# Performance work log

Measured on AMD Instinct MI355X. Metric: run time of the kernel, lower is better.

The kernel has to match this reference:

```python
import jax, jax.numpy as jnp
import numpy as np
import math

D_IN = 1024
D_OUT = 1024
NUM_HEADS = 16
D_HEAD = D_IN // NUM_HEADS


def setup_inputs() -> dict:
    key = jax.random.key(0)
    k1, k2, k3 = jax.random.split(key, 3)
    x = jax.random.normal(k1, (4, 2048, D_IN), dtype=jnp.float32)
    W_qkv = jax.random.normal(k2, (D_IN, 3 * D_OUT), dtype=jnp.float32) * (1.0 / math.sqrt(D_IN))
    b_qkv = jax.random.normal(k3, (3 * D_OUT,), dtype=jnp.float32) * 0.01
    return {"x": x, "W_qkv": W_qkv, "b_qkv": b_qkv}


def reference(x, W_qkv, b_qkv):
    B, S, _ = x.shape
    H, Dh = NUM_HEADS, D_HEAD
    # QKV projection: [B, S, 3*d_out]
    qkv = jnp.einsum('bsd,de->bse', x, W_qkv) + b_qkv
    # reshape per original: (B, S, H, 3*Dh) -> (B, H, S, 3*Dh)
    qkv = qkv.reshape(B, S, H, 3 * Dh).transpose(0, 2, 1, 3)
    q, k, v = jnp.split(qkv, 3, axis=-1)  # each [B, H, S, Dh]
    scale = 1.0 / math.sqrt(Dh)
    scores = jnp.einsum('bhqd,bhkd->bhqk', q, k) * scale
    attn = jax.nn.softmax(scores, axis=-1)
    ctx = jnp.einsum('bhqk,bhkd->bhqd', attn, v)  # [B, H, S, Dh]
    # (B, H, S, Dh) -> (B, S, H*Dh)
    return ctx.transpose(0, 2, 1, 3).reshape(B, S, D_OUT)
```

## Files before the change

kernel.cpp:

```cpp
#include <hip/hip_runtime.h>
#include <stdint.h>
#include <math.h>

#define D_IN   1024
#define NQKV   3072
#define NHEADS 16
#define DH     64
#define BATCH  4
#define SEQ    2048
#define MTOT   (BATCH*SEQ)

typedef __bf16    bf16x8 __attribute__((ext_vector_type(8)));
typedef _Float16  f16x8  __attribute__((ext_vector_type(8)));
typedef float     f32x4  __attribute__((ext_vector_type(4)));

__device__ __forceinline__ unsigned short f2bf(float f) {
    union { float f; uint32_t u; } c; c.f = f;
    uint32_t u = c.u;
    uint32_t r = u + 0x7fffu + ((u >> 16) & 1u);
    return (unsigned short)(r >> 16);
}
__device__ __forceinline__ float bf2f(unsigned short b) {
    union { uint32_t u; float f; } c; c.u = ((uint32_t)b) << 16;
    return c.f;
}
__device__ __forceinline__ uint32_t pkh(float a, float b) {
    auto h = __builtin_amdgcn_cvt_pkrtz(a, b);
    uint32_t u;
    __builtin_memcpy(&u, &h, 4);
    return u;
}

__global__ void k_convert_x(const float* __restrict__ x, unsigned short* __restrict__ xb) {
    int i = blockIdx.x * 256 + threadIdx.x;
    float4 v = ((const float4*)x)[i];
    ushort4 o;
    o.x = f2bf(v.x); o.y = f2bf(v.y); o.z = f2bf(v.z); o.w = f2bf(v.w);
    ((ushort4*)xb)[i] = o;
}

__global__ void k_convert_wt(const float* __restrict__ W, unsigned short* __restrict__ Wt) {
    __shared__ float tile[32][33];
    int tx = threadIdx.x, ty = threadIdx.y;
    int n0 = blockIdx.x * 32, k0 = blockIdx.y * 32;
    #pragma unroll
    for (int i = 0; i < 4; ++i) {
        int k = k0 + ty + i*8;
        tile[ty + i*8][tx] = W[(size_t)k * NQKV + n0 + tx];
    }
    __syncthreads();
    #pragma unroll
    for (int i = 0; i < 4; ++i) {
        int n = n0 + ty + i*8;
        Wt[(size_t)n * D_IN + k0 + tx] = f2bf(tile[tx][ty + i*8]);
    }
}

__global__ __launch_bounds__(256) void k_gemm_qkv(
    const unsigned short* __restrict__ A,
    const unsigned short* __restrict__ Bt,
    const float* __restrict__ bias,
    unsigned short* __restrict__ C)
{
    __shared__ __align__(16) unsigned short As[128*40];
    __shared__ __align__(16) unsigned short Bs[128*40];
    const int t = threadIdx.x;
    const int wave = t >> 6, lane = t & 63, quad = lane >> 4, l15 = lane & 15;
    const int wm = wave >> 1, wn = wave & 1;
    const int m0 = blockIdx.y * 128, n0 = blockIdx.x * 128;

    f32x4 acc[4][4] = {};

    for (int k0 = 0; k0 < D_IN; k0 += 32) {
        __syncthreads();
        #pragma unroll
        for (int i = 0; i < 2; ++i) {
            int idx = t + i*256;
            int row = idx >> 2, c = (idx & 3) << 3;
            *(uint4*)(&As[row*40 + c]) = *(const uint4*)(&A [(size_t)(m0+row)*D_IN + k0 + c]);
            *(uint4*)(&Bs[row*40 + c]) = *(const uint4*)(&Bt[(size_t)(n0+row)*D_IN + k0 + c]);
        }
        __syncthreads();
        bf16x8 a[4], b[4];
        #pragma unroll
        for (int tm = 0; tm < 4; ++tm)
            a[tm] = *(const bf16x8*)(&As[(wm*64 + tm*16 + l15)*40 + quad*8]);
        #pragma unroll
        for (int tn = 0; tn < 4; ++tn)
            b[tn] = *(const bf16x8*)(&Bs[(wn*64 + tn*16 + l15)*40 + quad*8]);
        #pragma unroll
        for (int tm = 0; tm < 4; ++tm)
            #pragma unroll
            for (int tn = 0; tn < 4; ++tn)
                acc[tm][tn] = __builtin_amdgcn_mfma_f32_16x16x32_bf16(a[tm], b[tn], acc[tm][tn], 0, 0, 0);
    }
    #pragma unroll
    for (int tn = 0; tn < 4; ++tn) {
        int col = n0 + wn*64 + tn*16 + l15;
        float bv = bias[col];
        #pragma unroll
        for (int tm = 0; tm < 4; ++tm) {
            #pragma unroll
            for (int r = 0; r < 4; ++r) {
                int row = m0 + wm*64 + tm*16 + quad*4 + r;
                C[(size_t)row*NQKV + col] = f2bf(acc[tm][tn][r] + bv);
            }
        }
    }
}

#define TP 66
__global__ __launch_bounds__(256) void k_transpose_v(
    const unsigned short* __restrict__ qkv,
    unsigned short* __restrict__ vtg)
{
    __shared__ unsigned short T[64*TP];
    const int t = threadIdx.x;
    const int bh = blockIdx.y, b = bh >> 4, h = bh & 15;
    const int s0 = blockIdx.x * 64;
    const unsigned short* src = qkv + (size_t)(b*SEQ + s0)*NQKV + h*(3*DH) + 2*DH;
    #pragma unroll
    for (int i = 0; i < 2; ++i) {
        int idx = t + i*256;
        int s = idx >> 3, c = (idx & 7) << 3;
        uint4 v = *(const uint4*)(src + (size_t)s*NQKV + c);
        unsigned short* dst = &T[s*TP + c];
        const unsigned short* pv = (const unsigned short*)&v;
        #pragma unroll
        for (int j = 0; j < 8; ++j) {
            _Float16 hv = (_Float16)bf2f(pv[j]);
            dst[j] = *(unsigned short*)&hv;
        }
    }
    __syncthreads();
    unsigned short* out = vtg + (size_t)bh * DH * SEQ + s0;
    #pragma unroll
    for (int i = 0; i < 16; ++i) {
        int idx = t + i*256;
        int d = idx >> 6, s = idx & 63;
        out[(size_t)d * SEQ + s] = T[s*TP + d];
    }
}

#define PPAD 40
#define OPAD 72
__global__ __launch_bounds__(256, 2) void k_attn(
    const unsigned short* __restrict__ qkv,
    const unsigned short* __restrict__ vtg,
    float* __restrict__ out)
{
    __shared__ __align__(16) unsigned short Pl[4*64*PPAD];
    __shared__ __align__(16) unsigned short Os[4*64*OPAD];
    __shared__ float Lp[4*64];

    const int t = threadIdx.x;
    const int wave = t >> 6, lane = t & 63, quad = lane >> 4, l15 = lane & 15;
    const int bh = blockIdx.y, b = bh >> 4, h = bh & 15;
    const int m0 = blockIdx.x * 64;
    const unsigned short* base  = qkv + (size_t)(b*SEQ)*NQKV + h*(3*DH);
    const unsigned short* kbase = base + DH;
    const unsigned short* vbase = vtg + (size_t)bh * DH * SEQ;

    bf16x8 qb[4][2];
    #pragma unroll
    for (int tq = 0; tq < 4; ++tq) {
        const unsigned short* qrow = base + (size_t)(m0 + tq*16 + l15) * NQKV;
        qb[tq][0] = *(const bf16x8*)(qrow + quad*8);
        qb[tq][1] = *(const bf16x8*)(qrow + 32 + quad*8);
    }

    f32x4 o[4][4] = {};
    float lp[4] = {0.f, 0.f, 0.f, 0.f};
    unsigned short* pw = &Pl[wave*64*PPAD];
    const float c = 0.125f * 1.44269504089f;

    bf16x8 kf[2][2][2];
    f16x8  vf[2][4];
    {
        int key0 = wave*32;
        #pragma unroll
        for (int tk = 0; tk < 2; ++tk) {
            const unsigned short* kr = kbase + (size_t)(key0 + tk*16 + l15)*NQKV;
            kf[0][tk][0] = *(const bf16x8*)(kr + quad*8);
            kf[0][tk][1] = *(const bf16x8*)(kr + 32 + quad*8);
        }
        #pragma unroll
        for (int td = 0; td < 4; ++td)
            vf[0][td] = *(const f16x8*)(vbase + (size_t)(td*16 + l15)*SEQ + key0 + quad*8);
    }

    #pragma unroll 2
    for (int it = 0; it < 16; ++it) {
        const int cur = it & 1, nxt = cur ^ 1;
        if (it < 15) {
            int key0 = (it+1)*128 + wave*32;
            #pragma unroll
            for (int tk = 0; tk < 2; ++tk) {
                const unsigned short* kr = kbase + (size_t)(key0 + tk*16 + l15)*NQKV;
                kf[nxt][tk][0] = *(const bf16x8*)(kr + quad*8);
                kf[nxt][tk][1] = *(const bf16x8*)(kr + 32 + quad*8);
            }
            #pragma unroll
            for (int td = 0; td < 4; ++td)
                vf[nxt][td] = *(const f16x8*)(vbase + (size_t)(td*16 + l15)*SEQ + key0 + quad*8);
        }
        #pragma unroll
        for (int tk = 0; tk < 2; ++tk) {
            #pragma unroll
            for (int tq = 0; tq < 4; ++tq) {
                f32x4 a = {};
                a = __builtin_amdgcn_mfma_f32_16x16x32_bf16(kf[cur][tk][0], qb[tq][0], a, 0, 0, 0);
                a = __builtin_amdgcn_mfma_f32_16x16x32_bf16(kf[cur][tk][1], qb[tq][1], a, 0, 0, 0);
                float p0 = exp2f(a[0]*c), p1 = exp2f(a[1]*c);
                float p2 = exp2f(a[2]*c), p3 = exp2f(a[3]*c);
                lp[tq] += (p0 + p1) + (p2 + p3);
                uint2 u; u.x = pkh(p0, p1); u.y = pkh(p2, p3);
                *(uint2*)(&pw[(tq*16 + l15)*PPAD + tk*16 + quad*4]) = u;
            }
        }
        f16x8 pb[4];
        #pragma unroll
        for (int tq = 0; tq < 4; ++tq)
            pb[tq] = *(const f16x8*)(&pw[(tq*16 + l15)*PPAD + quad*8]);
        #pragma unroll
        for (int td = 0; td < 4; ++td)
            #pragma unroll
            for (int tq = 0; tq < 4; ++tq)
                o[td][tq] = __builtin_amdgcn_mfma_f32_16x16x32_f16(vf[cur][td], pb[tq], o[td][tq], 0, 0, 0);
    }

    {
        unsigned short* ow = &Os[wave*64*OPAD];
        #pragma unroll
        for (int td = 0; td < 4; ++td)
            #pragma unroll
            for (int tq = 0; tq < 4; ++tq) {
                uint2 u; u.x = pkh(o[td][tq][0], o[td][tq][1]); u.y = pkh(o[td][tq][2], o[td][tq][3]);
                *(uint2*)(&ow[(tq*16 + l15)*OPAD + td*16 + quad*4]) = u;
            }
        #pragma unroll
        for (int tq = 0; tq < 4; ++tq) {
            float s = lp[tq];
            s += __shfl_xor(s, 16);
            s += __shfl_xor(s, 32);
            if (quad == 0) Lp[wave*64 + tq*16 + l15] = s;
        }
    }
    __syncthreads();
    float* outb = out + (size_t)(b*SEQ + m0) * (NHEADS*DH) + h*DH;
    #pragma unroll
    for (int i = 0; i < 16; ++i) {
        int idx = t + i*256;
        int q = idx >> 6, d = idx & 63;
        float lt = Lp[q] + Lp[64 + q] + Lp[128 + q] + Lp[192 + q];
        float s = 0.f;
        #pragma unroll
        for (int w2 = 0; w2 < 4; ++w2) {
            _Float16 hv = *(const _Float16*)&Os[(w2*64 + q)*OPAD + d];
            s += (float)hv;
        }
        outb[(size_t)q * (NHEADS*DH) + d] = s / lt;
    }
}

extern "C" void kernel_launch(void* const* d_in, const int* in_sizes, int n_in,
                              void* d_out, int out_size, void* d_ws, size_t ws_size,
                              hipStream_t stream) {
    const float* x    = (const float*)d_in[0];
    const float* W    = (const float*)d_in[1];
    const float* bias = (const float*)d_in[2];
    float* out = (float*)d_out;

    unsigned short* xb  = (unsigned short*)d_ws;
    unsigned short* Wt  = xb  + (size_t)MTOT * D_IN;
    unsigned short* qkv = Wt  + (size_t)NQKV * D_IN;
    unsigned short* vtg = xb;

    hipLaunchKernelGGL(k_convert_x,   dim3(MTOT*D_IN/4/256), dim3(256),    0, stream, x, xb);
    hipLaunchKernelGGL(k_convert_wt,  dim3(NQKV/32, D_IN/32), dim3(32, 8), 0, stream, W, Wt);
    hipLaunchKernelGGL(k_gemm_qkv,    dim3(NQKV/128, MTOT/128), dim3(256), 0, stream, xb, Wt, bias, qkv);
    hipLaunchKernelGGL(k_transpose_v, dim3(SEQ/64, BATCH*NHEADS), dim3(256), 0, stream, qkv, vtg);
    hipLaunchKernelGGL(k_attn,        dim3(SEQ/64, BATCH*NHEADS), dim3(256), 0, stream, qkv, vtg, out);
}
```

Before: 319.8 us.

## Use direct global-to-LDS loads in QKV GEMM, fold softmax scale, raise attention occupancy

The QKV GEMM now stages A and B tiles with global_load_lds, which writes straight into an unpadded LDS layout and skips the register round-trip. The softmax scale and log2e factor are folded into Q during the GEMM epilogue, so the attention kernel drops one multiply per score. The attention kernel merges its P and O scratch buffers into one LDS array, adding a barrier so P is no longer in use before O overwrites it. It also raises launch bounds to 4 blocks per CU to increase occupancy, at the risk of register spills. Removing the LDS padding may cause bank conflicts on the fragment reads, and Q is now rounded to bf16 after scaling, which slightly changes precision.

```diff
diff --git a/kernel.cpp b/kernel.cpp
--- a/kernel.cpp
+++ b/kernel.cpp
@@ -14,6 +14,9 @@
 typedef _Float16  f16x8  __attribute__((ext_vector_type(8)));
 typedef float     f32x4  __attribute__((ext_vector_type(4)));
 
+typedef __attribute__((address_space(3))) unsigned short       lds_us;
+typedef __attribute__((address_space(1))) const unsigned short glb_us;
+
 __device__ __forceinline__ unsigned short f2bf(float f) {
     union { float f; uint32_t u; } c; c.f = f;
     uint32_t u = c.u;
@@ -62,48 +65,55 @@
     const float* __restrict__ bias,
     unsigned short* __restrict__ C)
 {
-    __shared__ __align__(16) unsigned short As[128*40];
-    __shared__ __align__(16) unsigned short Bs[128*40];
+    __shared__ __align__(16) unsigned short As[128*32];
+    __shared__ __align__(16) unsigned short Bs[128*32];
     const int t = threadIdx.x;
     const int wave = t >> 6, lane = t & 63, quad = lane >> 4, l15 = lane & 15;
     const int wm = wave >> 1, wn = wave & 1;
     const int m0 = blockIdx.y * 128, n0 = blockIdx.x * 128;
+    const int crow = lane >> 2;
+    const int ccol = (lane & 3) << 3;
 
     f32x4 acc[4][4] = {};
+    lds_us* As3 = (lds_us*)As;
+    lds_us* Bs3 = (lds_us*)Bs;
 
     for (int k0 = 0; k0 < D_IN; k0 += 32) {
-        __syncthreads();
-        #pragma unroll
-        for (int i = 0; i < 2; ++i) {
-            int idx = t + i*256;
-            int row = idx >> 2, c = (idx & 3) << 3;
-            *(uint4*)(&As[row*40 + c]) = *(const uint4*)(&A [(size_t)(m0+row)*D_IN + k0 + c]);
-            *(uint4*)(&Bs[row*40 + c]) = *(const uint4*)(&Bt[(size_t)(n0+row)*D_IN + k0 + c]);
+        #pragma unroll
+        for (int j = 0; j < 2; ++j) {
+            int chunk = wave*2 + j;
+            const unsigned short* ga = A  + (size_t)(m0 + chunk*16 + crow)*D_IN + k0 + ccol;
+            const unsigned short* gb = Bt + (size_t)(n0 + chunk*16 + crow)*D_IN + k0 + ccol;
+            __builtin_amdgcn_global_load_lds((glb_us*)ga, As3 + chunk*512, 16, 0, 0);
+            __builtin_amdgcn_global_load_lds((glb_us*)gb, Bs3 + chunk*512, 16, 0, 0);
         }
         __syncthreads();
         bf16x8 a[4], b[4];
         #pragma unroll
         for (int tm = 0; tm < 4; ++tm)
-            a[tm] = *(const bf16x8*)(&As[(wm*64 + tm*16 + l15)*40 + quad*8]);
+            a[tm] = *(const bf16x8*)(&As[(wm*64 + tm*16 + l15)*32 + quad*8]);
         #pragma unroll
         for (int tn = 0; tn < 4; ++tn)
-            b[tn] = *(const bf16x8*)(&Bs[(wn*64 + tn*16 + l15)*40 + quad*8]);
+            b[tn] = *(const bf16x8*)(&Bs[(wn*64 + tn*16 + l15)*32 + quad*8]);
         #pragma unroll
         for (int tm = 0; tm < 4; ++tm)
             #pragma unroll
             for (int tn = 0; tn < 4; ++tn)
                 acc[tm][tn] = __builtin_amdgcn_mfma_f32_16x16x32_bf16(a[tm], b[tn], acc[tm][tn], 0, 0, 0);
-    }
+        __syncthreads();
+    }
+    const float qs = 0.125f * 1.44269504089f;
     #pragma unroll
     for (int tn = 0; tn < 4; ++tn) {
         int col = n0 + wn*64 + tn*16 + l15;
         float bv = bias[col];
+        float s = ((col % 192) < 64) ? qs : 1.0f;
         #pragma unroll
         for (int tm = 0; tm < 4; ++tm) {
             #pragma unroll
             for (int r = 0; r < 4; ++r) {
                 int row = m0 + wm*64 + tm*16 + quad*4 + r;
-                C[(size_t)row*NQKV + col] = f2bf(acc[tm][tn][r] + bv);
+                C[(size_t)row*NQKV + col] = f2bf((acc[tm][tn][r] + bv) * s);
             }
         }
     }
@@ -144,13 +154,12 @@
 
 #define PPAD 40
 #define OPAD 72
-__global__ __launch_bounds__(256, 2) void k_attn(
+__global__ __launch_bounds__(256, 4) void k_attn(
     const unsigned short* __restrict__ qkv,
     const unsigned short* __restrict__ vtg,
     float* __restrict__ out)
 {
-    __shared__ __align__(16) unsigned short Pl[4*64*PPAD];
-    __shared__ __align__(16) unsigned short Os[4*64*OPAD];
+    __shared__ __align__(16) unsigned short PO[4*64*OPAD];
     __shared__ float Lp[4*64];
 
     const int t = threadIdx.x;
@@ -171,8 +180,7 @@
 
     f32x4 o[4][4] = {};
     float lp[4] = {0.f, 0.f, 0.f, 0.f};
-    unsigned short* pw = &Pl[wave*64*PPAD];
-    const float c = 0.125f * 1.44269504089f;
+    unsigned short* pw = &PO[wave*64*PPAD];
 
     bf16x8 kf[2][2][2];
     f16x8  vf[2][4];
@@ -211,8 +219,8 @@
                 f32x4 a = {};
                 a = __builtin_amdgcn_mfma_f32_16x16x32_bf16(kf[cur][tk][0], qb[tq][0], a, 0, 0, 0);
                 a = __builtin_amdgcn_mfma_f32_16x16x32_bf16(kf[cur][tk][1], qb[tq][1], a, 0, 0, 0);
-                float p0 = exp2f(a[0]*c), p1 = exp2f(a[1]*c);
-                float p2 = exp2f(a[2]*c), p3 = exp2f(a[3]*c);
+                float p0 = exp2f(a[0]), p1 = exp2f(a[1]);
+                float p2 = exp2f(a[2]), p3 = exp2f(a[3]);
                 lp[tq] += (p0 + p1) + (p2 + p3);
                 uint2 u; u.x = pkh(p0, p1); u.y = pkh(p2, p3);
                 *(uint2*)(&pw[(tq*16 + l15)*PPAD + tk*16 + quad*4]) = u;
@@ -229,8 +237,16 @@
                 o[td][tq] = __builtin_amdgcn_mfma_f32_16x16x32_f16(vf[cur][td], pb[tq], o[td][tq], 0, 0, 0);
     }
 
+    #pragma unroll
+    for (int tq = 0; tq < 4; ++tq) {
+        float s = lp[tq];
+        s += __shfl_xor(s, 16);
+        s += __shfl_xor(s, 32);
+        if (quad == 0) Lp[wave*64 + tq*16 + l15] = s;
+    }
+    __syncthreads();
     {
-        unsigned short* ow = &Os[wave*64*OPAD];
+        unsigned short* ow = &PO[wave*64*OPAD];
         #pragma unroll
         for (int td = 0; td < 4; ++td)
             #pragma unroll
@@ -238,13 +254,6 @@
                 uint2 u; u.x = pkh(o[td][tq][0], o[td][tq][1]); u.y = pkh(o[td][tq][2], o[td][tq][3]);
                 *(uint2*)(&ow[(tq*16 + l15)*OPAD + td*16 + quad*4]) = u;
             }
-        #pragma unroll
-        for (int tq = 0; tq < 4; ++tq) {
-            float s = lp[tq];
-            s += __shfl_xor(s, 16);
-            s += __shfl_xor(s, 32);
-            if (quad == 0) Lp[wave*64 + tq*16 + l15] = s;
-        }
     }
     __syncthreads();
     float* outb = out + (size_t)(b*SEQ + m0) * (NHEADS*DH) + h*DH;
@@ -256,7 +265,7 @@
         float s = 0.f;
         #pragma unroll
         for (int w2 = 0; w2 < 4; ++w2) {
-            _Float16 hv = *(const _Float16*)&Os[(w2*64 + q)*OPAD + d];
+            _Float16 hv = *(const _Float16*)&PO[(w2*64 + q)*OPAD + d];
             s += (float)hv;
         }
         outb[(size_t)q * (NHEADS*DH) + d] = s / lt;
```

After: 921.1 us. 2.88x slower.
